# Kernel optimization log

Hardware: AMD Instinct MI355X
Metric: run time of the kernel (lower is better)

Reference implementation:

```python
import jax, jax.numpy as jnp
import numpy as np


def setup_inputs() -> dict:
    key = jax.random.key(0)
    B, C, L = 32, 64, 8192
    x = jax.random.normal(key, (B, C, L), dtype=jnp.float32)
    return {"x": x, "kernel_size": 9}


def reference(x, kernel_size):
    # Sliding-window median along the last (time) axis with replicate padding,
    # matching nn.ReplicationPad1d + Unfold + torch.median (lower median; k is odd
    # so it is the exact median = k//2-th order statistic).
    k = kernel_size
    p = (k - 1) // 2
    L = x.shape[-1]
    xp = jnp.pad(x, ((0, 0), (0, 0), (p, p)), mode="edge")  # [B, C, L + k - 1]
    # Stack the k shifted views -> [B, C, L, k] (k is a small static constant)
    win = jnp.stack([xp[:, :, i:i + L] for i in range(k)], axis=-1)
    return jnp.sort(win, axis=-1)[..., k // 2]
```

## Files before the change

### kernel.cpp

```cpp
#include <hip/hip_runtime.h>


#define TILE 1024
#define BLOCK 256
#define HALO 4

__device__ __forceinline__ void sort3(float a, float b, float c,
                                      float& lo, float& md, float& hi) {
    lo = fminf(fminf(a, b), c);
    hi = fmaxf(fmaxf(a, b), c);
    md = __builtin_amdgcn_fmed3f(a, b, c);
}

__device__ __forceinline__ float med9(const float* p) {
    float l0, m0, h0, l1, m1, h1, l2, m2, h2;
    sort3(p[0], p[1], p[2], l0, m0, h0);
    sort3(p[3], p[4], p[5], l1, m1, h1);
    sort3(p[6], p[7], p[8], l2, m2, h2);
    float lo = fmaxf(fmaxf(l0, l1), l2);
    float md = __builtin_amdgcn_fmed3f(m0, m1, m2);
    float hi = fminf(fminf(h0, h1), h2);
    return __builtin_amdgcn_fmed3f(lo, md, hi);
}

__global__ __launch_bounds__(BLOCK) void median9_kernel(
    const float* __restrict__ x, float* __restrict__ out, int L, int tilesPerRow) {
    __shared__ __align__(16) float s[TILE + 2 * HALO];

    const int tid = threadIdx.x;
    const int row = blockIdx.x / tilesPerRow;
    const int tile_start = (blockIdx.x % tilesPerRow) * TILE;
    const long long row_base = (long long)row * L;
    const float* xr = x + row_base;

    float4 v = ((const float4*)(xr + tile_start))[tid];
    ((float4*)(s + HALO))[tid] = v;

    if (tid < 2 * HALO) {
        int pos, sidx;
        if (tid < HALO) {
            pos = tile_start - HALO + tid;
            sidx = tid;
        } else {
            pos = tile_start + TILE + (tid - HALO);
            sidx = TILE + HALO + (tid - HALO);
        }
        pos = min(max(pos, 0), L - 1);
        s[sidx] = xr[pos];
    }
    __syncthreads();

    const float4* sv = (const float4*)(s + 4 * tid);
    float4 a = sv[0], b = sv[1], c = sv[2];
    float w[12] = {a.x, a.y, a.z, a.w,
                   b.x, b.y, b.z, b.w,
                   c.x, c.y, c.z, c.w};
    float4 r;
    r.x = med9(w + 0);
    r.y = med9(w + 1);
    r.z = med9(w + 2);
    r.w = med9(w + 3);

    ((float4*)(out + row_base + tile_start))[tid] = r;
}

extern "C" void kernel_launch(void* const* d_in, const int* in_sizes, int n_in,
                              void* d_out, int out_size, void* d_ws, size_t ws_size,
                              hipStream_t stream) {
    const float* x = (const float*)d_in[0];
    float* out = (float*)d_out;
    const int L = 8192;
    const int rows = in_sizes[0] / L;
    const int tilesPerRow = L / TILE;
    const int nblocks = rows * tilesPerRow;
    median9_kernel<<<nblocks, BLOCK, 0, stream>>>(x, out, L, tilesPerRow);
}
```

Baseline: 113.3 us.

## Load median windows directly from global memory and use nontemporal stores

Removes the shared-memory staging tile and the block barrier. Each thread now reads its 12-element window straight from global memory with three overlapping vector loads, falling back to clamped scalar loads only at row edges. Output is written with a nontemporal store to limit cache pollution. In exchange, global load traffic triples, though the overlapping reads between neighbouring threads should mostly hit in cache.

```diff
diff --git a/kernel.cpp b/kernel.cpp
--- a/kernel.cpp
+++ b/kernel.cpp
@@ -4,6 +4,8 @@
 #define TILE 1024
 #define BLOCK 256
 #define HALO 4
+
+typedef float floatx4 __attribute__((ext_vector_type(4)));
 
 __device__ __forceinline__ void sort3(float a, float b, float c,
                                       float& lo, float& md, float& hi) {
@@ -25,43 +27,36 @@
 
 __global__ __launch_bounds__(BLOCK) void median9_kernel(
     const float* __restrict__ x, float* __restrict__ out, int L, int tilesPerRow) {
-    __shared__ __align__(16) float s[TILE + 2 * HALO];
-
     const int tid = threadIdx.x;
     const int row = blockIdx.x / tilesPerRow;
-    const int tile_start = (blockIdx.x % tilesPerRow) * TILE;
+    const int g = (blockIdx.x % tilesPerRow) * TILE + 4 * tid;
     const long long row_base = (long long)row * L;
     const float* xr = x + row_base;
 
-    float4 v = ((const float4*)(xr + tile_start))[tid];
-    ((float4*)(s + HALO))[tid] = v;
+    float w[12];
 
-    if (tid < 2 * HALO) {
-        int pos, sidx;
-        if (tid < HALO) {
-            pos = tile_start - HALO + tid;
-            sidx = tid;
-        } else {
-            pos = tile_start + TILE + (tid - HALO);
-            sidx = TILE + HALO + (tid - HALO);
+    if (g >= HALO && g + 2 * HALO <= L) {
+        const floatx4* p = (const floatx4*)(xr + g - HALO);
+        floatx4 a = p[0], b = p[1], c = p[2];
+        w[0] = a.x; w[1] = a.y; w[2]  = a.z; w[3]  = a.w;
+        w[4] = b.x; w[5] = b.y; w[6]  = b.z; w[7]  = b.w;
+        w[8] = c.x; w[9] = c.y; w[10] = c.z; w[11] = c.w;
+    } else {
+#pragma unroll
+        for (int j = 0; j < 12; ++j) {
+            int pos = g - HALO + j;
+            pos = min(max(pos, 0), L - 1);
+            w[j] = xr[pos];
         }
-        pos = min(max(pos, 0), L - 1);
-        s[sidx] = xr[pos];
     }
-    __syncthreads();
 
-    const float4* sv = (const float4*)(s + 4 * tid);
-    float4 a = sv[0], b = sv[1], c = sv[2];
-    float w[12] = {a.x, a.y, a.z, a.w,
-                   b.x, b.y, b.z, b.w,
-                   c.x, c.y, c.z, c.w};
-    float4 r;
+    floatx4 r;
     r.x = med9(w + 0);
     r.y = med9(w + 1);
     r.z = med9(w + 2);
     r.w = med9(w + 3);
 
-    ((float4*)(out + row_base + tile_start))[tid] = r;
+    __builtin_nontemporal_store(r, (floatx4*)(out + row_base + g));
 }
 
 extern "C" void kernel_launch(void* const* d_in, const int* in_sizes, int n_in,
```

Measured after the change: 109.0 us. 1.04x faster.
